# Kernel optimization log

Hardware: AMD Instinct MI355X
Metric: run time of the kernel (lower is better)

The kernel has to match this reference:

```python
import jax, jax.numpy as jnp
import numpy as np

N, F, H, O, D = 4096, 128, 4, 64, 64


def setup_inputs() -> dict:
    key = jax.random.key(0)
    k1, k2, k3, k4, k5 = jax.random.split(key, 5)
    h = jax.random.normal(k1, (1, N, F), dtype=jnp.float32)
    # dense binary adjacency (0/1)
    a = jax.random.randint(k2, (1, N, N), 0, 2).astype(jnp.float32)
    kernel = jax.random.normal(k3, (H, F, O), dtype=jnp.float32) * 0.1
    attn_kernel = jax.random.normal(k4, (H, F, D), dtype=jnp.float32) * 0.1
    attn_kernel2 = jax.random.normal(k5, (H, F, D), dtype=jnp.float32) * 0.1
    return {"h": h, "a": a, "kernel": kernel, "attn_kernel": attn_kernel, "attn_kernel2": attn_kernel2}


def reference(h, a, kernel, attn_kernel, attn_kernel2):
    x = h[0]          # [N, F]
    adj = a[0]        # [N, N] dense 0/1 adjacency
    # per-head linear projections, vectorized over heads
    feats = jnp.einsum('nf,hfo->hno', x, kernel)          # [H, N, O]
    f_self = jnp.einsum('nf,hfd->hnd', x, attn_kernel)    # [H, N, D]
    f_other = jnp.einsum('nf,hfd->hnd', x, attn_kernel2)  # [H, N, D]
    # dense attention logits, masked BEFORE the nonlinearity (as in original)
    dense = jnp.einsum('hnd,hmd->hnm', f_self, f_other)   # [H, N, N]
    masked = adj[None] * dense
    masked = jnp.where(masked >= 0, masked, 0.2 * masked)  # LeakyReLU(0.2)
    masked = masked / jnp.sqrt(jnp.asarray(D, jnp.float32))
    neg_inf = jnp.where(adj == 0, jnp.float32(-1e9), jnp.float32(0.0))  # [N, N]
    att = jax.nn.softmax(masked + neg_inf[None], axis=-1)
    att = att * (adj != 0).astype(att.dtype)[None]
    # aggregation (dropout is identity at inference, rate=0)
    node_features = jnp.einsum('hnm,hmo->hno', att, feats)  # [H, N, O]
    node_features = jax.nn.relu(node_features)
    # zero out padding rows (all-zero input features)
    row_mask = (jnp.sum((x != 0).astype(jnp.float32), axis=-1, keepdims=True) > 0).astype(jnp.float32)  # [N, 1]
    node_features = node_features * row_mask[None]
    # concat heads along last dim -> [1, N, H*O]
    out = jnp.transpose(node_features, (1, 0, 2)).reshape(N, H * O)
    return out[None]
```

## Files before the change

### kernel.cpp

```cpp
#include <hip/hip_runtime.h>
#include <hip/hip_bf16.h>

typedef unsigned short u16;
typedef unsigned int u32;
typedef unsigned long long u64;
typedef __attribute__((ext_vector_type(8))) short bf16x8;
typedef __attribute__((ext_vector_type(4))) float f32x4;
typedef __attribute__((ext_vector_type(4))) u16 u16x4;

#define N 4096
#define F 128
#define H 4
#define O 64
#define NW (N / 64)
#define NT 16
#define QSCALE 0.18033688011112043f

__device__ inline float exp2_hw(float x) {
#if __has_builtin(__builtin_amdgcn_exp2f)
  return __builtin_amdgcn_exp2f(x);
#else
  return __expf(x * 0.6931471805599453f);
#endif
}

__device__ inline u16 f2bf(float f) {
  union { __hip_bfloat16 b; u16 u; } v;
  v.b = __float2bfloat16(f);
  return v.u;
}

__global__ __launch_bounds__(256) void proj_kernel(
    const float* __restrict__ x, const float* __restrict__ wv,
    const float* __restrict__ wq, const float* __restrict__ wk,
    u16* __restrict__ Q, u16* __restrict__ K, u16* __restrict__ Vt) {
  __shared__ float xs[64][132];
  __shared__ float wsh[128][64];
  const int t = threadIdx.x;
  const int brow = blockIdx.x * 64;
  const int p = blockIdx.y, h = p / 3, which = p % 3;
  const float* W = (which == 0 ? wq : which == 1 ? wk : wv) + h * F * O;

#pragma unroll
  for (int i = 0; i < 8; i++) {
    int idx = t + i * 256, r = idx >> 5, c4 = idx & 31;
    *(float4*)&xs[r][c4 * 4] = *(const float4*)&x[(brow + r) * F + c4 * 4];
  }
#pragma unroll
  for (int i = 0; i < 8; i++) {
    int idx = t + i * 256, r = idx >> 4, c4 = idx & 15;
    *(float4*)&wsh[r][c4 * 4] = *(const float4*)&W[r * O + c4 * 4];
  }
  __syncthreads();

  const int r0 = (t >> 4) << 2, c0 = (t & 15) << 2;
  float acc[4][4] = {};
#pragma unroll 8
  for (int f = 0; f < F; f++) {
    float4 b = *(float4*)&wsh[f][c0];
    float a0 = xs[r0 + 0][f], a1 = xs[r0 + 1][f];
    float a2 = xs[r0 + 2][f], a3 = xs[r0 + 3][f];
    acc[0][0] = fmaf(a0, b.x, acc[0][0]); acc[0][1] = fmaf(a0, b.y, acc[0][1]);
    acc[0][2] = fmaf(a0, b.z, acc[0][2]); acc[0][3] = fmaf(a0, b.w, acc[0][3]);
    acc[1][0] = fmaf(a1, b.x, acc[1][0]); acc[1][1] = fmaf(a1, b.y, acc[1][1]);
    acc[1][2] = fmaf(a1, b.z, acc[1][2]); acc[1][3] = fmaf(a1, b.w, acc[1][3]);
    acc[2][0] = fmaf(a2, b.x, acc[2][0]); acc[2][1] = fmaf(a2, b.y, acc[2][1]);
    acc[2][2] = fmaf(a2, b.z, acc[2][2]); acc[2][3] = fmaf(a2, b.w, acc[2][3]);
    acc[3][0] = fmaf(a3, b.x, acc[3][0]); acc[3][1] = fmaf(a3, b.y, acc[3][1]);
    acc[3][2] = fmaf(a3, b.z, acc[3][2]); acc[3][3] = fmaf(a3, b.w, acc[3][3]);
  }

  if (which == 0) {
    u16* dst = Q + h * N * O;
#pragma unroll
    for (int i = 0; i < 4; i++) {
      u16x4 v4 = { f2bf(acc[i][0] * QSCALE), f2bf(acc[i][1] * QSCALE),
                   f2bf(acc[i][2] * QSCALE), f2bf(acc[i][3] * QSCALE) };
      *(u16x4*)&dst[(brow + r0 + i) * O + c0] = v4;
    }
  } else if (which == 1) {
    u16* dst = K + h * N * O;
#pragma unroll
    for (int i = 0; i < 4; i++) {
      u16x4 v4 = { f2bf(acc[i][0]), f2bf(acc[i][1]), f2bf(acc[i][2]), f2bf(acc[i][3]) };
      *(u16x4*)&dst[(brow + r0 + i) * O + c0] = v4;
    }
  } else {
    u16* dst = Vt + h * O * N;
#pragma unroll
    for (int j = 0; j < 4; j++) {
      u16x4 v4 = { f2bf(acc[0][j]), f2bf(acc[1][j]), f2bf(acc[2][j]), f2bf(acc[3][j]) };
      *(u16x4*)&dst[(c0 + j) * N + brow + r0] = v4;
    }
  }
}

__global__ __launch_bounds__(256) void mask_kernel(const float* __restrict__ x,
                                                   float* __restrict__ mask) {
  int n = blockIdx.x * 256 + threadIdx.x;
  const float4* xr = (const float4*)(x + n * F);
  float s = 0.f;
#pragma unroll
  for (int i = 0; i < F / 4; i++) {
    float4 v = xr[i];
    s += fabsf(v.x) + fabsf(v.y) + fabsf(v.z) + fabsf(v.w);
  }
  mask[n] = (s != 0.f) ? 1.f : 0.f;
}

__global__ __launch_bounds__(256) void pack_kernel(const float* __restrict__ adj,
                                                   u64* __restrict__ bits) {
  const int w = threadIdx.x >> 6, l = threadIdx.x & 63;
  const int row = blockIdx.x * 4 + w;
  const float* ar = adj + (size_t)row * N;
  u64* br = bits + (size_t)row * NW;
#pragma unroll 4
  for (int j2 = 0; j2 < 16; j2++) {
    float4 v = *(const float4*)&ar[j2 * 256 + l * 4];
    unsigned nib = (unsigned)(v.x != 0.f) | ((unsigned)(v.y != 0.f) << 1) |
                   ((unsigned)(v.z != 0.f) << 2) | ((unsigned)(v.w != 0.f) << 3);
    u64 word = (u64)nib << ((l & 15) * 4);
    word |= __shfl_xor(word, 1);
    word |= __shfl_xor(word, 2);
    word |= __shfl_xor(word, 4);
    word |= __shfl_xor(word, 8);
    if ((l & 15) == 0) br[j2 * 4 + (l >> 4)] = word;
  }
}

__global__ __launch_bounds__(512) void attn_kernel(
    const u64* __restrict__ bits, const u16* __restrict__ Qg,
    const u16* __restrict__ Kg, const u16* __restrict__ Vtg,
    float* __restrict__ Opart, float* __restrict__ Spart) {
  __shared__ __align__(16) char kv[2][4][8192];
  __shared__ __align__(16) u16 pst[8][16][64];

  const int tid = threadIdx.x;
  const int w = tid >> 6, l = tid & 63;
  const int lm = l & 15, lg = l >> 4;
  const int rg = w >> 1, hc = w & 1;
  const int h = blockIdx.y;
  const int z = blockIdx.z;
  const int R0 = blockIdx.x * 64;
  const int WR0 = R0 + rg * 16;
  const int CB0 = z * 2048;

  const char* Kb = (const char*)(Kg + h * N * O);
  const char* Vb = (const char*)(Vtg + h * O * N);
  const u64* bblk = bits + (size_t)WR0 * NW;

  const int srow = w * 8 + (l >> 3);
  const int scol = ((l & 7) * 16) ^ ((srow & 7) << 4);

  const u16* Qh = Qg + h * N * O;
  bf16x8 qa0 = *(const bf16x8*)&Qh[(WR0 + lm) * O + lg * 8];
  bf16x8 qa1 = *(const bf16x8*)&Qh[(WR0 + lm) * O + 32 + lg * 8];

  f32x4 oacc[4];
  float lsum[4] = {0.f, 0.f, 0.f, 0.f};
#pragma unroll
  for (int i = 0; i < 4; i++) oacc[i] = (f32x4){0.f, 0.f, 0.f, 0.f};
  const f32x4 zero4 = {0.f, 0.f, 0.f, 0.f};

  auto STAGE = [&](int b, int t) {
    __builtin_amdgcn_global_load_lds(
        (const u32*)(Kb + (size_t)(CB0 + 0 * 1024 + t * 64 + srow) * 128 + scol),
        (u32*)&kv[b][0][w * 1024], 16, 0, 0);
    __builtin_amdgcn_global_load_lds(
        (const u32*)(Kb + (size_t)(CB0 + 1 * 1024 + t * 64 + srow) * 128 + scol),
        (u32*)&kv[b][1][w * 1024], 16, 0, 0);
    __builtin_amdgcn_global_load_lds(
        (const u32*)(Vb + (size_t)srow * (N * 2) + (CB0 + 0 * 1024 + t * 64) * 2 + scol),
        (u32*)&kv[b][2][w * 1024], 16, 0, 0);
    __builtin_amdgcn_global_load_lds(
        (const u32*)(Vb + (size_t)srow * (N * 2) + (CB0 + 1 * 1024 + t * 64) * 2 + scol),
        (u32*)&kv[b][3][w * 1024], 16, 0, 0);
  };

  STAGE(0, 0);
  __syncthreads();

  int b = 0;
#pragma unroll 1
  for (int t = 0; t < NT; ++t) {
    if (t + 1 < NT) STAGE(b ^ 1, t + 1);

    const int widx = (CB0 >> 6) + hc * NT + t;

    u64 sh0 = bblk[(lg * 4 + 0) * NW + widx] >> lm;
    u64 sh1 = bblk[(lg * 4 + 1) * NW + widx] >> lm;
    u64 sh2 = bblk[(lg * 4 + 2) * NW + widx] >> lm;
    u64 sh3 = bblk[(lg * 4 + 3) * NW + widx] >> lm;

    const char* Kt = &kv[b][hc][0];
    f32x4 sacc[4];
    __builtin_amdgcn_s_setprio(1);
#pragma unroll
    for (int tt = 0; tt < 4; tt++) {
      const int row = tt * 16 + lm;
      const int sw = (row & 7) << 4;
      bf16x8 kb0 = *(const bf16x8*)(Kt + row * 128 + ((lg * 16) ^ sw));
      bf16x8 kb1 = *(const bf16x8*)(Kt + row * 128 + ((lg * 16 + 64) ^ sw));
      f32x4 s0 = __builtin_amdgcn_mfma_f32_16x16x32_bf16(qa0, kb0, zero4, 0, 0, 0);
      sacc[tt] = __builtin_amdgcn_mfma_f32_16x16x32_bf16(qa1, kb1, s0, 0, 0, 0);
    }
    __builtin_amdgcn_s_setprio(0);

#pragma unroll
    for (int tt = 0; tt < 4; tt++) {
#pragma unroll
      for (int r = 0; r < 4; r++) {
        u64 sh = (r == 0 ? sh0 : r == 1 ? sh1 : r == 2 ? sh2 : sh3);
        unsigned bit = (unsigned)(sh >> (tt * 16)) & 1u;
        float sv = sacc[tt][r];
        float lv = (sv < 0.f ? 0.2f * sv : sv);
        float p = bit ? exp2_hw(lv) : 0.f;
        lsum[r] += p;
        pst[w][lg * 4 + r][tt * 16 + lm] = f2bf(p);
      }
    }
    bf16x8 pa0 = *(const bf16x8*)&pst[w][lm][lg * 8];
    bf16x8 pa1 = *(const bf16x8*)&pst[w][lm][32 + lg * 8];

    const char* Vt_ = &kv[b][2 + hc][0];
    __builtin_amdgcn_s_setprio(1);
#pragma unroll
    for (int ot = 0; ot < 4; ot++) {
      const int o = ot * 16 + lm;
      const int sw = (o & 7) << 4;
      bf16x8 vb0 = *(const bf16x8*)(Vt_ + o * 128 + ((lg * 16) ^ sw));
      bf16x8 vb1 = *(const bf16x8*)(Vt_ + o * 128 + ((lg * 16 + 64) ^ sw));
      oacc[ot] = __builtin_amdgcn_mfma_f32_16x16x32_bf16(pa0, vb0, oacc[ot], 0, 0, 0);
      oacc[ot] = __builtin_amdgcn_mfma_f32_16x16x32_bf16(pa1, vb1, oacc[ot], 0, 0, 0);
    }
    __builtin_amdgcn_s_setprio(0);

    __syncthreads();
    b ^= 1;
  }

#pragma unroll
  for (int r = 0; r < 4; r++) {
    float s = lsum[r];
    s += __shfl_xor(s, 1);
    s += __shfl_xor(s, 2);
    s += __shfl_xor(s, 4);
    s += __shfl_xor(s, 8);
    lsum[r] = s;
  }

  float (*Om2)[64][64] = (float (*)[64][64])&kv[0][0][0];
#pragma unroll
  for (int ot = 0; ot < 4; ot++)
#pragma unroll
    for (int r = 0; r < 4; r++)
      Om2[hc][rg * 16 + lg * 4 + r][ot * 16 + lm] = oacc[ot][r];
  if (lm == 0) {
    float* ps = (float*)&pst[w][0][0];
#pragma unroll
    for (int r = 0; r < 4; r++) ps[lg * 4 + r] = lsum[r];
  }
  __syncthreads();

  const int row = tid >> 3;
  const int c0 = (tid & 7) * 8;
  const int grow = R0 + row;
  float* op = &Opart[(((size_t)z * H + h) * N + grow) * O + c0];
#pragma unroll
  for (int j = 0; j < 8; j++)
    op[j] = Om2[0][row][c0 + j] + Om2[1][row][c0 + j];
  if ((tid & 7) == 0) {
    const int rg2 = row >> 4, ri = row & 15;
    float s0 = ((float*)&pst[rg2 * 2 + 0][0][0])[ri];
    float s1 = ((float*)&pst[rg2 * 2 + 1][0][0])[ri];
    Spart[((size_t)z * H + h) * N + grow] = s0 + s1;
  }
}

__global__ __launch_bounds__(256) void merge_kernel(
    const float* __restrict__ Opart, const float* __restrict__ Spart,
    const float* __restrict__ rowmask, float* __restrict__ out) {
  const int h = blockIdx.y;
  const int idx = blockIdx.x * 256 + threadIdx.x;
  const int row = idx >> 4, c0 = (idx & 15) * 4;
  float S = Spart[(size_t)h * N + row] + Spart[((size_t)H + h) * N + row];
  float inv = (S > 0.f) ? 1.f / S : 0.f;
  float rm = rowmask[row];
  const float4 o0 = *(const float4*)&Opart[((size_t)h * N + row) * O + c0];
  const float4 o1 = *(const float4*)&Opart[(((size_t)H + h) * N + row) * O + c0];
  float4 r;
  r.x = fmaxf((o0.x + o1.x) * inv, 0.f) * rm;
  r.y = fmaxf((o0.y + o1.y) * inv, 0.f) * rm;
  r.z = fmaxf((o0.z + o1.z) * inv, 0.f) * rm;
  r.w = fmaxf((o0.w + o1.w) * inv, 0.f) * rm;
  *(float4*)&out[(size_t)row * (H * O) + h * O + c0] = r;
}

extern "C" void kernel_launch(void* const* d_in, const int* in_sizes, int n_in,
                              void* d_out, int out_size, void* d_ws, size_t ws_size,
                              hipStream_t stream) {
  const float* x   = (const float*)d_in[0];
  const float* adj = (const float*)d_in[1];
  const float* wv  = (const float*)d_in[2];
  const float* wq  = (const float*)d_in[3];
  const float* wk  = (const float*)d_in[4];
  float* out = (float*)d_out;

  u16* Q  = (u16*)d_ws;
  u16* K  = Q + H * N * O;
  u16* Vt = K + H * N * O;
  float* rmask = (float*)(Vt + H * N * O);
  u64* bits = (u64*)(rmask + N);
  float* Opart = (float*)(bits + (size_t)N * NW);
  float* Spart = Opart + (size_t)2 * H * N * O;

  proj_kernel<<<dim3(N / 64, 12), 256, 0, stream>>>(x, wv, wq, wk, Q, K, Vt);
  mask_kernel<<<dim3(N / 256), 256, 0, stream>>>(x, rmask);
  pack_kernel<<<dim3(N / 4), 256, 0, stream>>>(adj, bits);
  attn_kernel<<<dim3(N / 64, H, 2), 512, 0, stream>>>(bits, Q, K, Vt, Opart, Spart);
  merge_kernel<<<dim3(N * O / 4 / 256, H), 256, 0, stream>>>(Opart, Spart, rmask, out);
}
```

Baseline: 83.51 us.

## Fuse projection, mask and adjacency packing into one prep kernel; swizzle P staging

Merges the three preprocessing kernels (adjacency bit-packing, QKV projection, row-mask) into a single launch whose blocks are split by index range, removing two kernel launches and letting the independent stages overlap on the GPU. Separately, the per-wave P tile in shared memory is now written and read with an XOR swizzle to cut LDS bank conflicts on the scatter store and the bf16x8 reads. The fused kernel carries the projection's shared-memory footprint in every block, which may lower occupancy for the packing blocks.

Measured after the change: 77.08 us. 7.7% less time.

```diff
diff --git a/kernel.cpp b/kernel.cpp
--- a/kernel.cpp
+++ b/kernel.cpp
@@ -30,101 +30,101 @@
   return v.u;
 }
 
-__global__ __launch_bounds__(256) void proj_kernel(
-    const float* __restrict__ x, const float* __restrict__ wv,
-    const float* __restrict__ wq, const float* __restrict__ wk,
-    u16* __restrict__ Q, u16* __restrict__ K, u16* __restrict__ Vt) {
-  __shared__ float xs[64][132];
-  __shared__ float wsh[128][64];
+__global__ __launch_bounds__(256) void prep_kernel(
+    const float* __restrict__ x, const float* __restrict__ adj,
+    const float* __restrict__ wv, const float* __restrict__ wq,
+    const float* __restrict__ wk, u16* __restrict__ Q, u16* __restrict__ K,
+    u16* __restrict__ Vt, float* __restrict__ rmask, u64* __restrict__ bits) {
+  const int b = blockIdx.x;
   const int t = threadIdx.x;
-  const int brow = blockIdx.x * 64;
-  const int p = blockIdx.y, h = p / 3, which = p % 3;
-  const float* W = (which == 0 ? wq : which == 1 ? wk : wv) + h * F * O;
-
-#pragma unroll
-  for (int i = 0; i < 8; i++) {
-    int idx = t + i * 256, r = idx >> 5, c4 = idx & 31;
-    *(float4*)&xs[r][c4 * 4] = *(const float4*)&x[(brow + r) * F + c4 * 4];
-  }
-#pragma unroll
-  for (int i = 0; i < 8; i++) {
-    int idx = t + i * 256, r = idx >> 4, c4 = idx & 15;
-    *(float4*)&wsh[r][c4 * 4] = *(const float4*)&W[r * O + c4 * 4];
-  }
-  __syncthreads();
-
-  const int r0 = (t >> 4) << 2, c0 = (t & 15) << 2;
-  float acc[4][4] = {};
+
+  if (b < 1024) {
+    const int w = t >> 6, l = t & 63;
+    const int row = b * 4 + w;
+    const float* ar = adj + (size_t)row * N;
+    u64* br = bits + (size_t)row * NW;
+#pragma unroll 4
+    for (int j2 = 0; j2 < 16; j2++) {
+      float4 v = *(const float4*)&ar[j2 * 256 + l * 4];
+      unsigned nib = (unsigned)(v.x != 0.f) | ((unsigned)(v.y != 0.f) << 1) |
+                     ((unsigned)(v.z != 0.f) << 2) | ((unsigned)(v.w != 0.f) << 3);
+      u64 word = (u64)nib << ((l & 15) * 4);
+      word |= __shfl_xor(word, 1);
+      word |= __shfl_xor(word, 2);
+      word |= __shfl_xor(word, 4);
+      word |= __shfl_xor(word, 8);
+      if ((l & 15) == 0) br[j2 * 4 + (l >> 4)] = word;
+    }
+  } else if (b < 1792) {
+    __shared__ float xs[64][132];
+    __shared__ float wsh[128][64];
+    const int pb = b - 1024;
+    const int brow = (pb & 63) * 64;
+    const int p = pb >> 6, h = p / 3, which = p % 3;
+    const float* W = (which == 0 ? wq : which == 1 ? wk : wv) + h * F * O;
+
+#pragma unroll
+    for (int i = 0; i < 8; i++) {
+      int idx = t + i * 256, r = idx >> 5, c4 = idx & 31;
+      *(float4*)&xs[r][c4 * 4] = *(const float4*)&x[(brow + r) * F + c4 * 4];
+    }
+#pragma unroll
+    for (int i = 0; i < 8; i++) {
+      int idx = t + i * 256, r = idx >> 4, c4 = idx & 15;
+      *(float4*)&wsh[r][c4 * 4] = *(const float4*)&W[r * O + c4 * 4];
+    }
+    __syncthreads();
+
+    const int r0 = (t >> 4) << 2, c0 = (t & 15) << 2;
+    float acc[4][4] = {};
 #pragma unroll 8
-  for (int f = 0; f < F; f++) {
-    float4 b = *(float4*)&wsh[f][c0];
-    float a0 = xs[r0 + 0][f], a1 = xs[r0 + 1][f];
-    float a2 = xs[r0 + 2][f], a3 = xs[r0 + 3][f];
-    acc[0][0] = fmaf(a0, b.x, acc[0][0]); acc[0][1] = fmaf(a0, b.y, acc[0][1]);
-    acc[0][2] = fmaf(a0, b.z, acc[0][2]); acc[0][3] = fmaf(a0, b.w, acc[0][3]);
-    acc[1][0] = fmaf(a1, b.x, acc[1][0]); acc[1][1] = fmaf(a1, b.y, acc[1][1]);
-    acc[1][2] = fmaf(a1, b.z, acc[1][2]); acc[1][3] = fmaf(a1, b.w, acc[1][3]);
-    acc[2][0] = fmaf(a2, b.x, acc[2][0]); acc[2][1] = fmaf(a2, b.y, acc[2][1]);
-    acc[2][2] = fmaf(a2, b.z, acc[2][2]); acc[2][3] = fmaf(a2, b.w, acc[2][3]);
-    acc[3][0] = fmaf(a3, b.x, acc[3][0]); acc[3][1] = fmaf(a3, b.y, acc[3][1]);
-    acc[3][2] = fmaf(a3, b.z, acc[3][2]); acc[3][3] = fmaf(a3, b.w, acc[3][3]);
-  }
-
-  if (which == 0) {
-    u16* dst = Q + h * N * O;
-#pragma unroll
-    for (int i = 0; i < 4; i++) {
-      u16x4 v4 = { f2bf(acc[i][0] * QSCALE), f2bf(acc[i][1] * QSCALE),
-                   f2bf(acc[i][2] * QSCALE), f2bf(acc[i][3] * QSCALE) };
-      *(u16x4*)&dst[(brow + r0 + i) * O + c0] = v4;
-    }
-  } else if (which == 1) {
-    u16* dst = K + h * N * O;
-#pragma unroll
-    for (int i = 0; i < 4; i++) {
-      u16x4 v4 = { f2bf(acc[i][0]), f2bf(acc[i][1]), f2bf(acc[i][2]), f2bf(acc[i][3]) };
-      *(u16x4*)&dst[(brow + r0 + i) * O + c0] = v4;
+    for (int f = 0; f < F; f++) {
+      float4 bb = *(float4*)&wsh[f][c0];
+      float a0 = xs[r0 + 0][f], a1 = xs[r0 + 1][f];
+      float a2 = xs[r0 + 2][f], a3 = xs[r0 + 3][f];
+      acc[0][0] = fmaf(a0, bb.x, acc[0][0]); acc[0][1] = fmaf(a0, bb.y, acc[0][1]);
+      acc[0][2] = fmaf(a0, bb.z, acc[0][2]); acc[0][3] = fmaf(a0, bb.w, acc[0][3]);
+      acc[1][0] = fmaf(a1, bb.x, acc[1][0]); acc[1][1] = fmaf(a1, bb.y, acc[1][1]);
+      acc[1][2] = fmaf(a1, bb.z, acc[1][2]); acc[1][3] = fmaf(a1, bb.w, acc[1][3]);
+      acc[2][0] = fmaf(a2, bb.x, acc[2][0]); acc[2][1] = fmaf(a2, bb.y, acc[2][1]);
+      acc[2][2] = fmaf(a2, bb.z, acc[2][2]); acc[2][3] = fmaf(a2, bb.w, acc[2][3]);
+      acc[3][0] = fmaf(a3, bb.x, acc[3][0]); acc[3][1] = fmaf(a3, bb.y, acc[3][1]);
+      acc[3][2] = fmaf(a3, bb.z, acc[3][2]); acc[3][3] = fmaf(a3, bb.w, acc[3][3]);
+    }
+
+    if (which == 0) {
+      u16* dst = Q + h * N * O;
+#pragma unroll
+      for (int i = 0; i < 4; i++) {
+        u16x4 v4 = { f2bf(acc[i][0] * QSCALE), f2bf(acc[i][1] * QSCALE),
+                     f2bf(acc[i][2] * QSCALE), f2bf(acc[i][3] * QSCALE) };
+        *(u16x4*)&dst[(brow + r0 + i) * O + c0] = v4;
+      }
+    } else if (which == 1) {
+      u16* dst = K + h * N * O;
+#pragma unroll
+      for (int i = 0; i < 4; i++) {
+        u16x4 v4 = { f2bf(acc[i][0]), f2bf(acc[i][1]), f2bf(acc[i][2]), f2bf(acc[i][3]) };
+        *(u16x4*)&dst[(brow + r0 + i) * O + c0] = v4;
+      }
+    } else {
+      u16* dst = Vt + h * O * N;
+#pragma unroll
+      for (int j = 0; j < 4; j++) {
+        u16x4 v4 = { f2bf(acc[0][j]), f2bf(acc[1][j]), f2bf(acc[2][j]), f2bf(acc[3][j]) };
+        *(u16x4*)&dst[(c0 + j) * N + brow + r0] = v4;
+      }
     }
   } else {
-    u16* dst = Vt + h * O * N;
-#pragma unroll
-    for (int j = 0; j < 4; j++) {
-      u16x4 v4 = { f2bf(acc[0][j]), f2bf(acc[1][j]), f2bf(acc[2][j]), f2bf(acc[3][j]) };
-      *(u16x4*)&dst[(c0 + j) * N + brow + r0] = v4;
-    }
-  }
-}
-
-__global__ __launch_bounds__(256) void mask_kernel(const float* __restrict__ x,
-                                                   float* __restrict__ mask) {
-  int n = blockIdx.x * 256 + threadIdx.x;
-  const float4* xr = (const float4*)(x + n * F);
-  float s = 0.f;
-#pragma unroll
-  for (int i = 0; i < F / 4; i++) {
-    float4 v = xr[i];
-    s += fabsf(v.x) + fabsf(v.y) + fabsf(v.z) + fabsf(v.w);
-  }
-  mask[n] = (s != 0.f) ? 1.f : 0.f;
-}
-
-__global__ __launch_bounds__(256) void pack_kernel(const float* __restrict__ adj,
-                                                   u64* __restrict__ bits) {
-  const int w = threadIdx.x >> 6, l = threadIdx.x & 63;
-  const int row = blockIdx.x * 4 + w;
-  const float* ar = adj + (size_t)row * N;
-  u64* br = bits + (size_t)row * NW;
-#pragma unroll 4
-  for (int j2 = 0; j2 < 16; j2++) {
-    float4 v = *(const float4*)&ar[j2 * 256 + l * 4];
-    unsigned nib = (unsigned)(v.x != 0.f) | ((unsigned)(v.y != 0.f) << 1) |
-                   ((unsigned)(v.z != 0.f) << 2) | ((unsigned)(v.w != 0.f) << 3);
-    u64 word = (u64)nib << ((l & 15) * 4);
-    word |= __shfl_xor(word, 1);
-    word |= __shfl_xor(word, 2);
-    word |= __shfl_xor(word, 4);
-    word |= __shfl_xor(word, 8);
-    if ((l & 15) == 0) br[j2 * 4 + (l >> 4)] = word;
+    int n = (b - 1792) * 256 + t;
+    const float4* xr = (const float4*)(x + n * F);
+    float s = 0.f;
+#pragma unroll
+    for (int i = 0; i < F / 4; i++) {
+      float4 v = xr[i];
+      s += fabsf(v.x) + fabsf(v.y) + fabsf(v.z) + fabsf(v.w);
+    }
+    rmask[n] = (s != 0.f) ? 1.f : 0.f;
   }
 }
 
@@ -155,6 +155,10 @@
   const u16* Qh = Qg + h * N * O;
   bf16x8 qa0 = *(const bf16x8*)&Qh[(WR0 + lm) * O + lg * 8];
   bf16x8 qa1 = *(const bf16x8*)&Qh[(WR0 + lm) * O + 32 + lg * 8];
+
+  char* pbase = (char*)&pst[w][0][0];
+  const char* prd0 = pbase + lm * 128 + ((lg * 16) ^ ((lm & 7) << 4));
+  const char* prd1 = pbase + lm * 128 + ((64 + lg * 16) ^ ((lm & 7) << 4));
 
   f32x4 oacc[4];
   float lsum[4] = {0.f, 0.f, 0.f, 0.f};
@@ -216,11 +220,13 @@
         float lv = (sv < 0.f ? 0.2f * sv : sv);
         float p = bit ? exp2_hw(lv) : 0.f;
         lsum[r] += p;
-        pst[w][lg * 4 + r][tt * 16 + lm] = f2bf(p);
+        const int prow = lg * 4 + r;
+        *(u16*)(pbase + prow * 128 +
+                ((((tt * 16 + lm) * 2)) ^ ((prow & 7) << 4))) = f2bf(p);
       }
     }
-    bf16x8 pa0 = *(const bf16x8*)&pst[w][lm][lg * 8];
-    bf16x8 pa1 = *(const bf16x8*)&pst[w][lm][32 + lg * 8];
+    bf16x8 pa0 = *(const bf16x8*)prd0;
+    bf16x8 pa1 = *(const bf16x8*)prd1;
 
     const char* Vt_ = &kv[b][2 + hc][0];
     __builtin_amdgcn_s_setprio(1);
@@ -256,7 +262,7 @@
     for (int r = 0; r < 4; r++)
       Om2[hc][rg * 16 + lg * 4 + r][ot * 16 + lm] = oacc[ot][r];
   if (lm == 0) {
-    float* ps = (float*)&pst[w][0][0];
+    float* ps = (float*)pbase;
 #pragma unroll
     for (int r = 0; r < 4; r++) ps[lg * 4 + r] = lsum[r];
   }
@@ -314,9 +320,7 @@
   float* Opart = (float*)(bits + (size_t)N * NW);
   float* Spart = Opart + (size_t)2 * H * N * O;
 
-  proj_kernel<<<dim3(N / 64, 12), 256, 0, stream>>>(x, wv, wq, wk, Q, K, Vt);
-  mask_kernel<<<dim3(N / 256), 256, 0, stream>>>(x, rmask);
-  pack_kernel<<<dim3(N / 4), 256, 0, stream>>>(adj, bits);
+  prep_kernel<<<dim3(1808), 256, 0, stream>>>(x, adj, wv, wq, wk, Q, K, Vt, rmask, bits);
   attn_kernel<<<dim3(N / 64, H, 2), 512, 0, stream>>>(bits, Q, K, Vt, Opart, Spart);
   merge_kernel<<<dim3(N * O / 4 / 256, H), 256, 0, stream>>>(Opart, Spart, rmask, out);
 }
```
